# Kernel optimization log

Hardware: AMD Instinct MI355X
Metric: run time of the kernel (lower is better)

Reference implementation:

```python
import jax, jax.numpy as jnp
import numpy as np

B, S, D = 4, 2048, 1024
H, HD = 16, 64  # n_heads, head_dim; D == H*HD


def setup_inputs() -> dict:
    key = jax.random.key(0)
    k1, k2, k3, k4, k5 = jax.random.split(key, 5)
    s = 0.02
    return {
        "x": jax.random.normal(k1, (B, S, D), dtype=jnp.float32),
        "w_qkv": jax.random.normal(k2, (D, 3 * D), dtype=jnp.float32) * s,
        "b_qkv": jax.random.normal(k3, (3 * D,), dtype=jnp.float32) * s,
        "w_out": jax.random.normal(k4, (D, D), dtype=jnp.float32) * s,
        "b_out": jax.random.normal(k5, (D,), dtype=jnp.float32) * s,
    }


def reference(x, w_qkv, b_qkv, w_out, b_out):
    b, s, d = x.shape
    qkv = x @ w_qkv + b_qkv                      # [B,S,3D]
    qkv = qkv.reshape(b, s, 3, H, HD)
    qkv = jnp.transpose(qkv, (2, 0, 3, 1, 4))    # [3,B,H,S,HD]
    q, k, v = qkv[0], qkv[1], qkv[2]
    scale = 1.0 / np.sqrt(HD).astype(np.float32)
    scores = jnp.einsum("bhqd,bhkd->bhqk", q, k) * scale  # [B,H,S,S]
    causal = jnp.tril(jnp.ones((s, s), dtype=bool))
    scores = jnp.where(causal[None, None], scores, -jnp.inf)
    weights = jax.nn.softmax(scores, axis=-1)
    attn = jnp.einsum("bhqk,bhkd->bhqd", weights, v)       # [B,H,S,HD]
    attn = jnp.transpose(attn, (0, 2, 1, 3)).reshape(b, s, d)
    return attn @ w_out + b_out
```

## Files before the change

kernel.cpp:

```cpp
#include <hip/hip_runtime.h>
#include <hip/hip_bf16.h>

#define B_DIM 4
#define S_DIM 2048
#define D_DIM 1024
#define H_DIM 16
#define HD_DIM 64

using bf16 = __hip_bfloat16;
using bf16x8 = __attribute__((ext_vector_type(8))) short;
using f32x4 = __attribute__((ext_vector_type(4))) float;

__device__ inline unsigned short f2bfu(float f) {
    bf16 h = __float2bfloat16(f);
    unsigned short s;
    __builtin_memcpy(&s, &h, 2);
    return s;
}
__device__ inline unsigned int pack2bf(float a, float b) {
    return (unsigned int)f2bfu(a) | ((unsigned int)f2bfu(b) << 16);
}
__device__ inline float exp2_raw(float x) {
    float r;
    asm("v_exp_f32 %0, %1" : "=v"(r) : "v"(x));
    return r;
}

typedef __attribute__((address_space(1))) const void cg_void;
typedef __attribute__((address_space(3))) void lds_void;
__device__ inline void gload_lds16(const void* g, void* l) {
    __builtin_amdgcn_global_load_lds((cg_void*)g, (lds_void*)l, 16, 0, 0);
}

__global__ __launch_bounds__(256) void prep_kernel(const float* __restrict__ x,
                                                   bf16* __restrict__ xb,
                                                   const float* __restrict__ wq,
                                                   bf16* __restrict__ wqT,
                                                   const float* __restrict__ wo,
                                                   bf16* __restrict__ woT) {
    int bid = blockIdx.x;
    int tid = threadIdx.x;
    if (bid < 8192) {
        int i = bid * 256 + tid;
        float4 v = reinterpret_cast<const float4*>(x)[i];
        ushort4 o;
        o.x = f2bfu(v.x); o.y = f2bfu(v.y); o.z = f2bfu(v.z); o.w = f2bfu(v.w);
        reinterpret_cast<ushort4*>(xb)[i] = o;
        return;
    }
    __shared__ float tile[32][33];
    const float* in;
    bf16* out;
    int R, C, bx, by;
    if (bid < 11264) {
        int loc = bid - 8192;
        in = wq; out = wqT; R = D_DIM; C = 3 * D_DIM;
        bx = loc % 96; by = loc / 96;
    } else {
        int loc = bid - 11264;
        in = wo; out = woT; R = D_DIM; C = D_DIM;
        bx = loc % 32; by = loc / 32;
    }
    int tx = tid & 31, ty = tid >> 5;
    int c0 = bx * 32, r0 = by * 32;
#pragma unroll
    for (int i = 0; i < 32; i += 8)
        tile[ty + i][tx] = in[(size_t)(r0 + ty + i) * C + c0 + tx];
    __syncthreads();
#pragma unroll
    for (int i = 0; i < 32; i += 8)
        out[(size_t)(c0 + ty + i) * R + r0 + tx] = __float2bfloat16(tile[tx][ty + i]);
}

#define GEMM_PRE(BN_)                                                          \
    const int K = D_DIM;                                                       \
    int bid3 = blockIdx.x;                                                     \
    int xcd = bid3 & 7;                                                        \
    int inner = bid3 >> 3;                                                     \
    int m0 = (xcd * 4 + (inner & 3)) * 256;                                    \
    int n0 = (inner >> 2) * (BN_);                                             \
    int tid = threadIdx.x;                                                     \
    int lane = tid & 63;                                                       \
    int w = tid >> 6;                                                          \
    int wr = w >> 1, wc = w & 1;                                               \
    int lr = lane & 15, lk = lane >> 4;                                        \
    int r = tid >> 3;                                                          \
    int cs = ((tid & 7) ^ (r & 7)) * 8;                                        \
    int wub = w * 1024;                                                        \
    const int rsw = (lr & 7) << 4;                                             \
    const bf16* Ag = A + (size_t)(m0 + r) * K + cs;                            \
    const bf16* Bg = BT + (size_t)(n0 + r) * K + cs;

#define STAGE_A4(buf, kt, BUF_)                                                \
    do {                                                                       \
        char* d_ = smem + (buf) * (BUF_) + wub;                                \
        gload_lds16(Ag + (kt) * 64, d_);                                       \
        gload_lds16(Ag + 64 * 1024 + (kt) * 64, d_ + 8192);                    \
        gload_lds16(Ag + 128 * 1024 + (kt) * 64, d_ + 16384);                  \
        gload_lds16(Ag + 192 * 1024 + (kt) * 64, d_ + 24576);                  \
    } while (0)

#define STAGE_B3(buf, kt, BUF_)                                                \
    do {                                                                       \
        char* d_ = smem + (buf) * (BUF_) + 32768 + wub;                        \
        gload_lds16(Bg + (kt) * 64, d_);                                       \
        gload_lds16(Bg + 64 * 1024 + (kt) * 64, d_ + 8192);                    \
        gload_lds16(Bg + 128 * 1024 + (kt) * 64, d_ + 16384);                  \
    } while (0)

#define STAGE_B2(buf, kt, BUF_)                                                \
    do {                                                                       \
        char* d_ = smem + (buf) * (BUF_) + 32768 + wub;                        \
        gload_lds16(Bg + (kt) * 64, d_);                                       \
        gload_lds16(Bg + 64 * 1024 + (kt) * 64, d_ + 8192);                    \
    } while (0)

#define GEMM_MAIN(NF_, STAGE_B_, BUF_, W0_, W1_)                               \
    const int NT = K / 64;                                             \
    STAGE_B_(0, 0, BUF_);                                                      \
    STAGE_A4(0, 0, BUF_);                                                      \
    bf16x8 af0[4], af1[4], bf0[NF_], bf1[NF_], pa1[4], pb1[NF_];               \
    for (int t = 0; t < NT; ++t) {                                             \
        char* bufb = smem + (t & 1) * (BUF_);                                  \
        asm volatile("s_waitcnt " W0_ ::: "memory");                           \
        __builtin_amdgcn_s_barrier();                                          \
        __builtin_amdgcn_sched_barrier(0);                                     \
        _Pragma("unroll")                                                      \
        for (int nf = 0; nf < NF_; ++nf) {                                     \
            int row = wc * (NF_ * 16) + nf * 16 + lr;                          \
            char* ba = bufb + 32768 + row * 128;                               \
            bf0[nf] = *(const bf16x8*)(ba + ((lk * 16) ^ rsw));                \
            bf1[nf] = *(const bf16x8*)(ba + ((64 + lk * 16) ^ rsw));           \
        }                                                                      \
        if (t + 1 < NT) STAGE_B_((t + 1) & 1, t + 1, BUF_);                    \
        if (t) {                                                               \
            __builtin_amdgcn_s_setprio(1);                                     \
            _Pragma("unroll")                                                  \
            for (int mf = 0; mf < 4; ++mf)                                     \
                _Pragma("unroll")                                              \
                for (int nf = 0; nf < NF_; ++nf)                               \
                    acc[mf][nf] = __builtin_amdgcn_mfma_f32_16x16x32_bf16(     \
                        pa1[mf], pb1[nf], acc[mf][nf], 0, 0, 0);               \
            __builtin_amdgcn_s_setprio(0);                                     \
        }                                                                      \
        if (t + 1 < NT) asm volatile("s_waitcnt " W1_ ::: "memory");           \
        else            asm volatile("s_waitcnt vmcnt(0)" ::: "memory");       \
        __builtin_amdgcn_s_barrier();                                          \
        __builtin_amdgcn_sched_barrier(0);                                     \
        _Pragma("unroll")                                                      \
        for (int mf = 0; mf < 4; ++mf) {                                       \
            int row = wr * 64 + mf * 16 + lr;                                  \
            char* aa = bufb + row * 128;                                       \
            af0[mf] = *(const bf16x8*)(aa + ((lk * 16) ^ rsw));                \
            af1[mf] = *(const bf16x8*)(aa + ((64 + lk * 16) ^ rsw));           \
        }                                                                      \
        if (t + 1 < NT) STAGE_A4((t + 1) & 1, t + 1, BUF_);                    \
        __builtin_amdgcn_s_setprio(1);                                         \
        _Pragma("unroll")                                                      \
        for (int mf = 0; mf < 4; ++mf)                                         \
            _Pragma("unroll")                                                  \
            for (int nf = 0; nf < NF_; ++nf)                                   \
                acc[mf][nf] = __builtin_amdgcn_mfma_f32_16x16x32_bf16(         \
                    af0[mf], bf0[nf], acc[mf][nf], 0, 0, 0);                   \
        __builtin_amdgcn_s_setprio(0);                                         \
        _Pragma("unroll")                                                      \
        for (int mf = 0; mf < 4; ++mf) pa1[mf] = af1[mf];                      \
        _Pragma("unroll")                                                      \
        for (int nf = 0; nf < NF_; ++nf) pb1[nf] = bf1[nf];                    \
    }                                                                          \
    _Pragma("unroll")                                                          \
    for (int mf = 0; mf < 4; ++mf)                                             \
        _Pragma("unroll")                                                      \
        for (int nf = 0; nf < NF_; ++nf)                                       \
            acc[mf][nf] = __builtin_amdgcn_mfma_f32_16x16x32_bf16(             \
                pa1[mf], pb1[nf], acc[mf][nf], 0, 0, 0);

__global__ __launch_bounds__(512, 2) void gemm_qkv_kernel(const bf16* __restrict__ A,
                                                          const bf16* __restrict__ BT,
                                                          const float* __restrict__ bias,
                                                          bf16* __restrict__ Qo,
                                                          bf16* __restrict__ Ko,
                                                          bf16* __restrict__ Vt) {
    __shared__ __align__(16) char smem[114688];
    f32x4 acc[4][6] = {};
    GEMM_PRE(192);
    GEMM_MAIN(6, STAGE_B3, 57344, "vmcnt(4)", "vmcnt(3)");
    const float QS = 0.18033688f;
#pragma unroll
    for (int mf = 0; mf < 4; ++mf) {
        int row = m0 + wr * 64 + mf * 16 + lk * 4;
        int b = row >> 11, s = row & 2047;
#pragma unroll
        for (int nf = 0; nf < 6; ++nf) {
            int cb = n0 + wc * 96 + nf * 16;
            int third = cb >> 10;
            int col = cb + lr;
            int rem = col & 1023;
            int h = rem >> 6, hd = rem & 63;
            float bv = bias[col];
            if (third == 0) {
#pragma unroll
                for (int i = 0; i < 4; ++i)
                    Qo[(((size_t)b * H_DIM + h) * S_DIM + s + i) * HD_DIM + hd] =
                        __float2bfloat16((acc[mf][nf][i] + bv) * QS);
            } else if (third == 1) {
#pragma unroll
                for (int i = 0; i < 4; ++i)
                    Ko[(((size_t)b * H_DIM + h) * S_DIM + s + i) * HD_DIM + hd] =
                        __float2bfloat16(acc[mf][nf][i] + bv);
            } else {
                uint2 d;
                d.x = pack2bf(acc[mf][nf][0] + bv, acc[mf][nf][1] + bv);
                d.y = pack2bf(acc[mf][nf][2] + bv, acc[mf][nf][3] + bv);
                *(uint2*)&Vt[(((size_t)b * H_DIM + h) * HD_DIM + hd) * S_DIM + s] = d;
            }
        }
    }
}

__global__ __launch_bounds__(256, 4) void attn_kernel(const bf16* __restrict__ Q,
                                                      const bf16* __restrict__ K,
                                                      const bf16* __restrict__ Vt,
                                                      bf16* __restrict__ Aout) {
    __shared__ __align__(16) char smem[40960];
    int bid = blockIdx.x;
    int bh = bid & 63;
    const int st_tbl[16] = {15, 14, 13, 12, 8, 9, 10, 11, 4, 5, 6, 7, 3, 2, 1, 0};
    int st = st_tbl[bid >> 6];
    int b = bh >> 4, h = bh & 15;
    int w = threadIdx.x >> 6;
    int lane = threadIdx.x & 63;
    int lr = lane & 15, lk = lane >> 4;

    const short* Qs = (const short*)(Q + (size_t)bh * S_DIM * HD_DIM);
    const short* Ks = (const short*)(K + (size_t)bh * S_DIM * HD_DIM);
    const short* Vs = (const short*)(Vt + (size_t)bh * HD_DIM * S_DIM);
    char* pb = smem + 32768 + w * 2048;
    const int sw = (lr & 7) << 4;

    int srow = w * 8 + (lane >> 3);
    int sblk = ((lane & 7) ^ (lane >> 3)) * 8;
    int wub = w * 1024;

    int q0w = st * 128 + w * 32;
    int nt = 2 * st + 2;
    int twl = 2 * st + ((w >> 1) & 1);

    bf16x8 qf[2][2];
#pragma unroll
    for (int qg = 0; qg < 2; ++qg)
#pragma unroll
        for (int c = 0; c < 2; ++c)
            qf[qg][c] = *(const bf16x8*)&Qs[(size_t)(q0w + qg * 16 + lr) * 64 + c * 32 + lk * 8];

    bf16x8 onesv;
#pragma unroll
    for (int z = 0; z < 8; ++z) onesv[z] = (short)0x3F80;

    f32x4 o[4][2] = {};
    f32x4 ol[2] = {};

    gload_lds16(Ks + (size_t)srow * 64 + sblk, smem + wub);
    gload_lds16(Ks + (size_t)(32 + srow) * 64 + sblk, smem + 4096 + wub);
    gload_lds16(Vs + (size_t)srow * S_DIM + sblk, smem + 16384 + wub);
    gload_lds16(Vs + (size_t)(32 + srow) * S_DIM + sblk, smem + 20480 + wub);

    for (int t = 0; t < nt; ++t) {
        int cur = t & 1;
        int kv0 = t * 64;
        __syncthreads();
        if (t + 1 < nt) {
            int kn = kv0 + 64;
            char* kd = smem + (cur ^ 1) * 8192;
            char* vd = smem + 16384 + (cur ^ 1) * 8192;
            gload_lds16(Ks + (size_t)(kn + srow) * 64 + sblk, kd + wub);
            gload_lds16(Ks + (size_t)(kn + 32 + srow) * 64 + sblk, kd + 4096 + wub);
            gload_lds16(Vs + (size_t)srow * S_DIM + kn + sblk, vd + wub);
            gload_lds16(Vs + (size_t)(32 + srow) * S_DIM + kn + sblk, vd + 4096 + wub);
        }
        if (t > twl) continue;
        char* kt = smem + cur * 8192;
        char* vt = smem + 16384 + cur * 8192;
        bool diag = (t == twl);
        int mhi = diag ? ((w & 1) ? 4 : 2) : 4;

        f32x4 s[4][2] = {};
        __builtin_amdgcn_s_setprio(1);
#pragma unroll
        for (int m = 0; m < 4; ++m) {
            if (m >= mhi) continue;
            int rb = (m * 16 + lr) * 128;
            bf16x8 ka = *(const bf16x8*)(kt + rb + ((lk * 16) ^ sw));
            bf16x8 kb2 = *(const bf16x8*)(kt + rb + ((64 + lk * 16) ^ sw));
            s[m][0] = __builtin_amdgcn_mfma_f32_16x16x32_bf16(ka, qf[0][0], s[m][0], 0, 0, 0);
            s[m][0] = __builtin_amdgcn_mfma_f32_16x16x32_bf16(kb2, qf[0][1], s[m][0], 0, 0, 0);
            s[m][1] = __builtin_amdgcn_mfma_f32_16x16x32_bf16(ka, qf[1][0], s[m][1], 0, 0, 0);
            s[m][1] = __builtin_amdgcn_mfma_f32_16x16x32_bf16(kb2, qf[1][1], s[m][1], 0, 0, 0);
        }
        __builtin_amdgcn_s_setprio(0);

        if (kv0 + 63 > q0w) {
#pragma unroll
            for (int m = 0; m < 4; ++m)
#pragma unroll
                for (int qg = 0; qg < 2; ++qg) {
                    int qq = q0w + qg * 16 + lr;
#pragma unroll
                    for (int i = 0; i < 4; ++i)
                        if (kv0 + m * 16 + lk * 4 + i > qq) s[m][qg][i] = -1e30f;
                }
        }

#pragma unroll
        for (int m = 0; m < 4; ++m)
#pragma unroll
            for (int qg = 0; qg < 2; ++qg)
#pragma unroll
                for (int i = 0; i < 4; ++i) s[m][qg][i] = exp2_raw(s[m][qg][i]);

        bf16x8 pf[2][2];
#pragma unroll
        for (int qg = 0; qg < 2; ++qg) {
#pragma unroll
            for (int m = 0; m < 4; ++m) {
                uint2 d;
                d.x = pack2bf(s[m][qg][0], s[m][qg][1]);
                d.y = pack2bf(s[m][qg][2], s[m][qg][3]);
                *(uint2*)(pb + lr * 128 + ((m * 32 + lk * 8) ^ sw)) = d;
            }
            pf[qg][0] = *(const bf16x8*)(pb + lr * 128 + ((lk * 16) ^ sw));
            pf[qg][1] = *(const bf16x8*)(pb + lr * 128 + ((64 + lk * 16) ^ sw));
        }

        __builtin_amdgcn_s_setprio(1);
#pragma unroll
        for (int m = 0; m < 4; ++m) {
            int rb = (m * 16 + lr) * 128;
            bf16x8 va = *(const bf16x8*)(vt + rb + ((lk * 16) ^ sw));
            bf16x8 vb2 = *(const bf16x8*)(vt + rb + ((64 + lk * 16) ^ sw));
            o[m][0] = __builtin_amdgcn_mfma_f32_16x16x32_bf16(va, pf[0][0], o[m][0], 0, 0, 0);
            o[m][0] = __builtin_amdgcn_mfma_f32_16x16x32_bf16(vb2, pf[0][1], o[m][0], 0, 0, 0);
            o[m][1] = __builtin_amdgcn_mfma_f32_16x16x32_bf16(va, pf[1][0], o[m][1], 0, 0, 0);
            o[m][1] = __builtin_amdgcn_mfma_f32_16x16x32_bf16(vb2, pf[1][1], o[m][1], 0, 0, 0);
        }
        ol[0] = __builtin_amdgcn_mfma_f32_16x16x32_bf16(onesv, pf[0][0], ol[0], 0, 0, 0);
        ol[0] = __builtin_amdgcn_mfma_f32_16x16x32_bf16(onesv, pf[0][1], ol[0], 0, 0, 0);
        ol[1] = __builtin_amdgcn_mfma_f32_16x16x32_bf16(onesv, pf[1][0], ol[1], 0, 0, 0);
        ol[1] = __builtin_amdgcn_mfma_f32_16x16x32_bf16(onesv, pf[1][1], ol[1], 0, 0, 0);
        __builtin_amdgcn_s_setprio(0);
    }

    short* op = (short*)Aout;
#pragma unroll
    for (int qg = 0; qg < 2; ++qg) {
        float inv = 1.0f / ol[qg][0];
        size_t orow = ((size_t)b * S_DIM + q0w + qg * 16 + lr) * D_DIM + h * 64;
#pragma unroll
        for (int m = 0; m < 4; ++m) {
            uint2 d;
            d.x = pack2bf(o[m][qg][0] * inv, o[m][qg][1] * inv);
            d.y = pack2bf(o[m][qg][2] * inv, o[m][qg][3] * inv);
            *(uint2*)(op + orow + m * 16 + lk * 4) = d;
        }
    }
}

__global__ __launch_bounds__(512, 2) void gemm_out_kernel(const bf16* __restrict__ A,
                                                          const bf16* __restrict__ BT,
                                                          const float* __restrict__ bias,
                                                          float* __restrict__ Out) {
    __shared__ __align__(16) char smem[98304];
    f32x4 acc[4][4] = {};
    GEMM_PRE(128);
    GEMM_MAIN(4, STAGE_B2, 49152, "vmcnt(4)", "vmcnt(2)");
#pragma unroll
    for (int mf = 0; mf < 4; ++mf) {
        int row = m0 + wr * 64 + mf * 16 + lk * 4;
#pragma unroll
        for (int nf = 0; nf < 4; ++nf) {
            int col = n0 + wc * 64 + nf * 16 + lr;
            float bv = bias[col];
#pragma unroll
            for (int i = 0; i < 4; ++i)
                Out[(size_t)(row + i) * D_DIM + col] = acc[mf][nf][i] + bv;
        }
    }
}

extern "C" void kernel_launch(void* const* d_in, const int* in_sizes, int n_in,
                              void* d_out, int out_size, void* d_ws, size_t ws_size,
                              hipStream_t stream) {
    const float* x = (const float*)d_in[0];
    const float* w_qkv = (const float*)d_in[1];
    const float* b_qkv = (const float*)d_in[2];
    const float* w_out = (const float*)d_in[3];
    const float* b_out = (const float*)d_in[4];
    float* out = (float*)d_out;

    char* ws = (char*)d_ws;
    const size_t SZ_X = (size_t)B_DIM * S_DIM * D_DIM * 2;
    const size_t SZ_WQKV = (size_t)D_DIM * 3 * D_DIM * 2;
    const size_t SZ_WOUT = (size_t)D_DIM * D_DIM * 2;
    bf16* xb = (bf16*)(ws);
    bf16* wqkvT = (bf16*)(ws + SZ_X);
    bf16* woutT = (bf16*)(ws + SZ_X + SZ_WQKV);
    bf16* Qb = (bf16*)(ws + SZ_X + SZ_WQKV + SZ_WOUT);
    bf16* Kb = (bf16*)(ws + SZ_X + SZ_WQKV + SZ_WOUT + SZ_X);
    bf16* Vtb = (bf16*)(ws + SZ_X + SZ_WQKV + SZ_WOUT + 2 * SZ_X);

    prep_kernel<<<12288, 256, 0, stream>>>(x, xb, w_qkv, wqkvT, w_out, woutT);
    gemm_qkv_kernel<<<512, 512, 0, stream>>>(xb, wqkvT, b_qkv, Qb, Kb, Vtb);
    attn_kernel<<<dim3(B_DIM * H_DIM * 16), 256, 0, stream>>>(Qb, Kb, Vtb, xb);
    gemm_out_kernel<<<256, 512, 0, stream>>>(xb, woutT, b_out, out);
}
```

Before: 130.3 us.

## Triple-buffer B tiles in QKV GEMM to prefetch two K-steps ahead

The QKV projection GEMM now keeps three LDS buffers for the weight (B) tiles and issues B loads two iterations ahead, while A stays double-buffered. The vmcnt waits are retuned to match the deeper prefetch, and the out-projection GEMM macro is inlined unchanged. This is meant to hide more global-load latency for the B operand, at the cost of more LDS (139 KB), which may reduce occupancy below the two-block launch bound.

Result: slower. 134.6 us (+3.3%).

```diff
diff --git a/kernel.cpp b/kernel.cpp
--- a/kernel.cpp
+++ b/kernel.cpp
@@ -91,100 +91,107 @@
     const bf16* Ag = A + (size_t)(m0 + r) * K + cs;                            \
     const bf16* Bg = BT + (size_t)(n0 + r) * K + cs;
 
-#define STAGE_A4(buf, kt, BUF_)                                                \
-    do {                                                                       \
-        char* d_ = smem + (buf) * (BUF_) + wub;                                \
-        gload_lds16(Ag + (kt) * 64, d_);                                       \
-        gload_lds16(Ag + 64 * 1024 + (kt) * 64, d_ + 8192);                    \
-        gload_lds16(Ag + 128 * 1024 + (kt) * 64, d_ + 16384);                  \
-        gload_lds16(Ag + 192 * 1024 + (kt) * 64, d_ + 24576);                  \
-    } while (0)
-
-#define STAGE_B3(buf, kt, BUF_)                                                \
-    do {                                                                       \
-        char* d_ = smem + (buf) * (BUF_) + 32768 + wub;                        \
-        gload_lds16(Bg + (kt) * 64, d_);                                       \
-        gload_lds16(Bg + 64 * 1024 + (kt) * 64, d_ + 8192);                    \
-        gload_lds16(Bg + 128 * 1024 + (kt) * 64, d_ + 16384);                  \
-    } while (0)
-
-#define STAGE_B2(buf, kt, BUF_)                                                \
-    do {                                                                       \
-        char* d_ = smem + (buf) * (BUF_) + 32768 + wub;                        \
-        gload_lds16(Bg + (kt) * 64, d_);                                       \
-        gload_lds16(Bg + 64 * 1024 + (kt) * 64, d_ + 8192);                    \
-    } while (0)
-
-#define GEMM_MAIN(NF_, STAGE_B_, BUF_, W0_, W1_)                               \
-    const int NT = K / 64;                                             \
-    STAGE_B_(0, 0, BUF_);                                                      \
-    STAGE_A4(0, 0, BUF_);                                                      \
-    bf16x8 af0[4], af1[4], bf0[NF_], bf1[NF_], pa1[4], pb1[NF_];               \
-    for (int t = 0; t < NT; ++t) {                                             \
-        char* bufb = smem + (t & 1) * (BUF_);                                  \
-        asm volatile("s_waitcnt " W0_ ::: "memory");                           \
-        __builtin_amdgcn_s_barrier();                                          \
-        __builtin_amdgcn_sched_barrier(0);                                     \
-        _Pragma("unroll")                                                      \
-        for (int nf = 0; nf < NF_; ++nf) {                                     \
-            int row = wc * (NF_ * 16) + nf * 16 + lr;                          \
-            char* ba = bufb + 32768 + row * 128;                               \
-            bf0[nf] = *(const bf16x8*)(ba + ((lk * 16) ^ rsw));                \
-            bf1[nf] = *(const bf16x8*)(ba + ((64 + lk * 16) ^ rsw));           \
-        }                                                                      \
-        if (t + 1 < NT) STAGE_B_((t + 1) & 1, t + 1, BUF_);                    \
-        if (t) {                                                               \
-            __builtin_amdgcn_s_setprio(1);                                     \
-            _Pragma("unroll")                                                  \
-            for (int mf = 0; mf < 4; ++mf)                                     \
-                _Pragma("unroll")                                              \
-                for (int nf = 0; nf < NF_; ++nf)                               \
-                    acc[mf][nf] = __builtin_amdgcn_mfma_f32_16x16x32_bf16(     \
-                        pa1[mf], pb1[nf], acc[mf][nf], 0, 0, 0);               \
-            __builtin_amdgcn_s_setprio(0);                                     \
-        }                                                                      \
-        if (t + 1 < NT) asm volatile("s_waitcnt " W1_ ::: "memory");           \
-        else            asm volatile("s_waitcnt vmcnt(0)" ::: "memory");       \
-        __builtin_amdgcn_s_barrier();                                          \
-        __builtin_amdgcn_sched_barrier(0);                                     \
-        _Pragma("unroll")                                                      \
-        for (int mf = 0; mf < 4; ++mf) {                                       \
-            int row = wr * 64 + mf * 16 + lr;                                  \
-            char* aa = bufb + row * 128;                                       \
-            af0[mf] = *(const bf16x8*)(aa + ((lk * 16) ^ rsw));                \
-            af1[mf] = *(const bf16x8*)(aa + ((64 + lk * 16) ^ rsw));           \
-        }                                                                      \
-        if (t + 1 < NT) STAGE_A4((t + 1) & 1, t + 1, BUF_);                    \
-        __builtin_amdgcn_s_setprio(1);                                         \
-        _Pragma("unroll")                                                      \
-        for (int mf = 0; mf < 4; ++mf)                                         \
-            _Pragma("unroll")                                                  \
-            for (int nf = 0; nf < NF_; ++nf)                                   \
-                acc[mf][nf] = __builtin_amdgcn_mfma_f32_16x16x32_bf16(         \
-                    af0[mf], bf0[nf], acc[mf][nf], 0, 0, 0);                   \
-        __builtin_amdgcn_s_setprio(0);                                         \
-        _Pragma("unroll")                                                      \
-        for (int mf = 0; mf < 4; ++mf) pa1[mf] = af1[mf];                      \
-        _Pragma("unroll")                                                      \
-        for (int nf = 0; nf < NF_; ++nf) pb1[nf] = bf1[nf];                    \
-    }                                                                          \
-    _Pragma("unroll")                                                          \
-    for (int mf = 0; mf < 4; ++mf)                                             \
-        _Pragma("unroll")                                                      \
-        for (int nf = 0; nf < NF_; ++nf)                                       \
-            acc[mf][nf] = __builtin_amdgcn_mfma_f32_16x16x32_bf16(             \
-                pa1[mf], pb1[nf], acc[mf][nf], 0, 0, 0);
-
 __global__ __launch_bounds__(512, 2) void gemm_qkv_kernel(const bf16* __restrict__ A,
                                                           const bf16* __restrict__ BT,
                                                           const float* __restrict__ bias,
                                                           bf16* __restrict__ Qo,
                                                           bf16* __restrict__ Ko,
                                                           bf16* __restrict__ Vt) {
-    __shared__ __align__(16) char smem[114688];
+    __shared__ __align__(16) char smem[139264];
     f32x4 acc[4][6] = {};
     GEMM_PRE(192);
-    GEMM_MAIN(6, STAGE_B3, 57344, "vmcnt(4)", "vmcnt(3)");
+
+#define QKV_STAGE_A(buf, kt)                                                   \
+    do {                                                                       \
+        char* d_ = smem + (buf) * 32768 + wub;                                 \
+        gload_lds16(Ag + (kt) * 64, d_);                                       \
+        gload_lds16(Ag + 64 * 1024 + (kt) * 64, d_ + 8192);                    \
+        gload_lds16(Ag + 128 * 1024 + (kt) * 64, d_ + 16384);                  \
+        gload_lds16(Ag + 192 * 1024 + (kt) * 64, d_ + 24576);                  \
+    } while (0)
+#define QKV_STAGE_B(buf, kt)                                                   \
+    do {                                                                       \
+        char* d_ = smem + 65536 + (buf) * 24576 + wub;                         \
+        gload_lds16(Bg + (kt) * 64, d_);                                       \
+        gload_lds16(Bg + 64 * 1024 + (kt) * 64, d_ + 8192);                    \
+        gload_lds16(Bg + 128 * 1024 + (kt) * 64, d_ + 16384);                  \
+    } while (0)
+
+    const int NT = K / 64;
+    QKV_STAGE_B(0, 0);
+    QKV_STAGE_A(0, 0);
+    QKV_STAGE_B(1, 1);
+
+    bf16x8 af0[4], af1[4], bf0[6], bf1[6], pa1[4], pb1[6];
+    int bbuf = 0;
+    for (int t = 0; t < NT; ++t) {
+        char* as = smem + (t & 1) * 32768;
+        char* bs = smem + 65536 + bbuf * 24576;
+        if (t + 1 < NT) asm volatile("s_waitcnt vmcnt(7)" ::: "memory");
+        else            asm volatile("s_waitcnt vmcnt(4)" ::: "memory");
+        __builtin_amdgcn_s_barrier();
+        __builtin_amdgcn_sched_barrier(0);
+#pragma unroll
+        for (int nf = 0; nf < 6; ++nf) {
+            int row = wc * 96 + nf * 16 + lr;
+            char* ba = bs + row * 128;
+            bf0[nf] = *(const bf16x8*)(ba + ((lk * 16) ^ rsw));
+            bf1[nf] = *(const bf16x8*)(ba + ((64 + lk * 16) ^ rsw));
+        }
+        if (t + 1 < NT) QKV_STAGE_A((t + 1) & 1, t + 1);
+        if (t + 2 < NT) {
+            int nb = bbuf + 2; if (nb >= 3) nb -= 3;
+            QKV_STAGE_B(nb, t + 2);
+        }
+        if (t) {
+            __builtin_amdgcn_s_setprio(1);
+#pragma unroll
+            for (int mf = 0; mf < 4; ++mf)
+#pragma unroll
+                for (int nf = 0; nf < 6; ++nf)
+                    acc[mf][nf] = __builtin_amdgcn_mfma_f32_16x16x32_bf16(
+                        pa1[mf], pb1[nf], acc[mf][nf], 0, 0, 0);
+            __builtin_amdgcn_s_setprio(0);
+        }
+        if (t + 3 <= NT) {
+            if (t + 3 < NT || t + 2 == NT - 1)
+                ;
+        }
+        if (t <= NT - 3)      asm volatile("s_waitcnt vmcnt(10)" ::: "memory");
+        else if (t == NT - 2) asm volatile("s_waitcnt vmcnt(7)" ::: "memory");
+        else                  asm volatile("s_waitcnt vmcnt(0)" ::: "memory");
+        __builtin_amdgcn_s_barrier();
+        __builtin_amdgcn_sched_barrier(0);
+#pragma unroll
+        for (int mf = 0; mf < 4; ++mf) {
+            int row = wr * 64 + mf * 16 + lr;
+            char* aa = as + row * 128;
+            af0[mf] = *(const bf16x8*)(aa + ((lk * 16) ^ rsw));
+            af1[mf] = *(const bf16x8*)(aa + ((64 + lk * 16) ^ rsw));
+        }
+        __builtin_amdgcn_s_setprio(1);
+#pragma unroll
+        for (int mf = 0; mf < 4; ++mf)
+#pragma unroll
+            for (int nf = 0; nf < 6; ++nf)
+                acc[mf][nf] = __builtin_amdgcn_mfma_f32_16x16x32_bf16(
+                    af0[mf], bf0[nf], acc[mf][nf], 0, 0, 0);
+        __builtin_amdgcn_s_setprio(0);
+#pragma unroll
+        for (int mf = 0; mf < 4; ++mf) pa1[mf] = af1[mf];
+#pragma unroll
+        for (int nf = 0; nf < 6; ++nf) pb1[nf] = bf1[nf];
+        ++bbuf; if (bbuf >= 3) bbuf = 0;
+    }
+#pragma unroll
+    for (int mf = 0; mf < 4; ++mf)
+#pragma unroll
+        for (int nf = 0; nf < 6; ++nf)
+            acc[mf][nf] = __builtin_amdgcn_mfma_f32_16x16x32_bf16(
+                pa1[mf], pb1[nf], acc[mf][nf], 0, 0, 0);
+#undef QKV_STAGE_A
+#undef QKV_STAGE_B
+
     const float QS = 0.18033688f;
 #pragma unroll
     for (int mf = 0; mf < 4; ++mf) {
@@ -372,7 +379,83 @@
     __shared__ __align__(16) char smem[98304];
     f32x4 acc[4][4] = {};
     GEMM_PRE(128);
-    GEMM_MAIN(4, STAGE_B2, 49152, "vmcnt(4)", "vmcnt(2)");
+
+#define OUT_STAGE_A(buf, kt)                                                   \
+    do {                                                                       \
+        char* d_ = smem + (buf) * 49152 + wub;                                 \
+        gload_lds16(Ag + (kt) * 64, d_);                                       \
+        gload_lds16(Ag + 64 * 1024 + (kt) * 64, d_ + 8192);                    \
+        gload_lds16(Ag + 128 * 1024 + (kt) * 64, d_ + 16384);                  \
+        gload_lds16(Ag + 192 * 1024 + (kt) * 64, d_ + 24576);                  \
+    } while (0)
+#define OUT_STAGE_B(buf, kt)                                                   \
+    do {                                                                       \
+        char* d_ = smem + (buf) * 49152 + 32768 + wub;                         \
+        gload_lds16(Bg + (kt) * 64, d_);                                       \
+        gload_lds16(Bg + 64 * 1024 + (kt) * 64, d_ + 8192);                    \
+    } while (0)
+
+    const int NT = K / 64;
+    OUT_STAGE_B(0, 0);
+    OUT_STAGE_A(0, 0);
+    bf16x8 af0[4], af1[4], bf0[4], bf1[4], pa1[4], pb1[4];
+    for (int t = 0; t < NT; ++t) {
+        char* bufb = smem + (t & 1) * 49152;
+        asm volatile("s_waitcnt vmcnt(4)" ::: "memory");
+        __builtin_amdgcn_s_barrier();
+        __builtin_amdgcn_sched_barrier(0);
+#pragma unroll
+        for (int nf = 0; nf < 4; ++nf) {
+            int row = wc * 64 + nf * 16 + lr;
+            char* ba = bufb + 32768 + row * 128;
+            bf0[nf] = *(const bf16x8*)(ba + ((lk * 16) ^ rsw));
+            bf1[nf] = *(const bf16x8*)(ba + ((64 + lk * 16) ^ rsw));
+        }
+        if (t + 1 < NT) OUT_STAGE_B((t + 1) & 1, t + 1);
+        if (t) {
+            __builtin_amdgcn_s_setprio(1);
+#pragma unroll
+            for (int mf = 0; mf < 4; ++mf)
+#pragma unroll
+                for (int nf = 0; nf < 4; ++nf)
+                    acc[mf][nf] = __builtin_amdgcn_mfma_f32_16x16x32_bf16(
+                        pa1[mf], pb1[nf], acc[mf][nf], 0, 0, 0);
+            __builtin_amdgcn_s_setprio(0);
+        }
+        if (t + 1 < NT) asm volatile("s_waitcnt vmcnt(2)" ::: "memory");
+        else            asm volatile("s_waitcnt vmcnt(0)" ::: "memory");
+        __builtin_amdgcn_s_barrier();
+        __builtin_amdgcn_sched_barrier(0);
+#pragma unroll
+        for (int mf = 0; mf < 4; ++mf) {
+            int row = wr * 64 + mf * 16 + lr;
+            char* aa = bufb + row * 128;
+            af0[mf] = *(const bf16x8*)(aa + ((lk * 16) ^ rsw));
+            af1[mf] = *(const bf16x8*)(aa + ((64 + lk * 16) ^ rsw));
+        }
+        if (t + 1 < NT) OUT_STAGE_A((t + 1) & 1, t + 1);
+        __builtin_amdgcn_s_setprio(1);
+#pragma unroll
+        for (int mf = 0; mf < 4; ++mf)
+#pragma unroll
+            for (int nf = 0; nf < 4; ++nf)
+                acc[mf][nf] = __builtin_amdgcn_mfma_f32_16x16x32_bf16(
+                    af0[mf], bf0[nf], acc[mf][nf], 0, 0, 0);
+        __builtin_amdgcn_s_setprio(0);
+#pragma unroll
+        for (int mf = 0; mf < 4; ++mf) pa1[mf] = af1[mf];
+#pragma unroll
+        for (int nf = 0; nf < 4; ++nf) pb1[nf] = bf1[nf];
+    }
+#pragma unroll
+    for (int mf = 0; mf < 4; ++mf)
+#pragma unroll
+        for (int nf = 0; nf < 4; ++nf)
+            acc[mf][nf] = __builtin_amdgcn_mfma_f32_16x16x32_bf16(
+                pa1[mf], pb1[nf], acc[mf][nf], 0, 0, 0);
+#undef OUT_STAGE_A
+#undef OUT_STAGE_B
+
 #pragma unroll
     for (int mf = 0; mf < 4; ++mf) {
         int row = m0 + wr * 64 + mf * 16 + lk * 4;
```
